# Performance work log

Measured on AMD Instinct MI355X. Metric: run time of the kernel, lower is better.

Reference implementation:

```python
import jax, jax.numpy as jnp
import numpy as np

B, S, H, D = 2, 2048, 16, 64

def setup_inputs() -> dict:
    key = jax.random.key(0)
    kq, kk, kv = jax.random.split(key, 3)
    query = jax.random.normal(kq, (B, S, H, D), dtype=jnp.float32)
    k_ = jax.random.normal(kk, (B, S, H, D), dtype=jnp.float32)
    v_ = jax.random.normal(kv, (B, S, H, D), dtype=jnp.float32)
    return {"query": query, "key": k_, "value": v_}

def reference(query, key, value):
    # AsyncLongContextAttention with world_size=1 degenerates to full
    # softmax attention over the global sequence (all2all / ring are
    # pure data movement). Defaults: causal=False, dropout_p=0.0,
    # softmax_scale = 1/sqrt(head_dim) (flash-attn convention).
    scale = 1.0 / jnp.sqrt(jnp.asarray(query.shape[-1], query.dtype))
    # scores: [B, H, Sq, Sk]
    scores = jnp.einsum("bqhd,bkhd->bhqk", query, key) * scale
    probs = jax.nn.softmax(scores, axis=-1)
    # out: [B, Sq, H, D]
    out = jnp.einsum("bhqk,bkhd->bqhd", probs, value)
    return out
```

## Files before the change

### kernel.cpp

```cpp
#include <hip/hip_runtime.h>
#include <math.h>

using half8  = __attribute__((ext_vector_type(8))) _Float16;
using half4  = __attribute__((ext_vector_type(4))) _Float16;
using fp16x2 = __attribute__((ext_vector_type(2))) __fp16;
using f32x4  = __attribute__((ext_vector_type(4))) float;

namespace {
constexpr int NB = 2, NS = 2048, NH = 16, ND = 64;
constexpr int QBLK = 128, KVBLK = 64;
constexpr int RS = NH * ND;
constexpr int NT = NS / KVBLK;
constexpr int NSTEP = NT / 2;
constexpr size_t TILEH = 4096;
constexpr size_t TILEB = TILEH * 2;
constexpr size_t SCR_HALFS = (size_t)NB * NH * NT * TILEH;

__device__ __forceinline__ int sidx(int row, int col) {
    return row * 64 + (col ^ (((row & 7) ^ ((row >> 3) & 7)) << 3));
}
__device__ __forceinline__ int kperm(int k) {
    return 16 * (2 * (k >> 5) + ((k >> 2) & 1)) + 4 * ((k >> 3) & 3) + (k & 3);
}
__device__ __forceinline__ float ex2(float x) {
#if __has_builtin(__builtin_amdgcn_exp2f)
    return __builtin_amdgcn_exp2f(x);
#else
    return exp2f(x);
#endif
}
__device__ __forceinline__ half8 pk8(const float4& a, const float4& b) {
    half8 r;
    fp16x2* h = (fp16x2*)&r;
    h[0] = __builtin_amdgcn_cvt_pkrtz(a.x, a.y);
    h[1] = __builtin_amdgcn_cvt_pkrtz(a.z, a.w);
    h[2] = __builtin_amdgcn_cvt_pkrtz(b.x, b.y);
    h[3] = __builtin_amdgcn_cvt_pkrtz(b.z, b.w);
    return r;
}
__device__ __forceinline__ half8 pk8s(const float4& a, const float4& b, float s) {
    half8 r;
    fp16x2* h = (fp16x2*)&r;
    h[0] = __builtin_amdgcn_cvt_pkrtz(a.x * s, a.y * s);
    h[1] = __builtin_amdgcn_cvt_pkrtz(a.z * s, a.w * s);
    h[2] = __builtin_amdgcn_cvt_pkrtz(b.x * s, b.y * s);
    h[3] = __builtin_amdgcn_cvt_pkrtz(b.z * s, b.w * s);
    return r;
}
__device__ __forceinline__ half8 pk8v(const float* v) {
    half8 r;
    fp16x2* h = (fp16x2*)&r;
    h[0] = __builtin_amdgcn_cvt_pkrtz(v[0], v[1]);
    h[1] = __builtin_amdgcn_cvt_pkrtz(v[2], v[3]);
    h[2] = __builtin_amdgcn_cvt_pkrtz(v[4], v[5]);
    h[3] = __builtin_amdgcn_cvt_pkrtz(v[6], v[7]);
    return r;
}
__device__ __forceinline__ half8 pkexp(const f32x4& a, const f32x4& b) {
    half8 r;
    fp16x2* h = (fp16x2*)&r;
    h[0] = __builtin_amdgcn_cvt_pkrtz(ex2(a[0]), ex2(a[1]));
    h[1] = __builtin_amdgcn_cvt_pkrtz(ex2(a[2]), ex2(a[3]));
    h[2] = __builtin_amdgcn_cvt_pkrtz(ex2(b[0]), ex2(b[1]));
    h[3] = __builtin_amdgcn_cvt_pkrtz(ex2(b[2]), ex2(b[3]));
    return r;
}
__device__ __forceinline__ void gld16(const void* g, void* l) {
    __builtin_amdgcn_global_load_lds(
        (const __attribute__((address_space(1))) void*)g,
        (__attribute__((address_space(3))) void*)l, 16, 0, 0);
}
}

__global__ __launch_bounds__(512)
void prep_kernel(const float* __restrict__ Kg, const float* __restrict__ Vg,
                 _Float16* __restrict__ Kscr, _Float16* __restrict__ Vscr) {
    const int t  = threadIdx.x;
    const int bh = blockIdx.x;
    const int kt = blockIdx.y;
    const int b  = bh >> 4;
    const int h  = bh & 15;
    const size_t tile = ((size_t)bh * NT + kt) * TILEH;

    {
        const int row = t >> 3;
        const int sc0 = (t & 7) * 8;
        const int m   = kperm(row);
        const int kg  = m >> 4, mlc = m & 15;
        const int ks  = sc0 >> 5, mlg = (sc0 >> 3) & 3;
        const float* kp = Kg + (size_t)(b * NS + kt * KVBLK + row) * RS + h * ND + sc0;
        Kscr[tile + ((ks * 4 + kg) * 64 + mlg * 16 + mlc) * 8 + 0];
        *(half8*)&Kscr[tile + (size_t)((ks * 4 + kg) * 64 + mlg * 16 + mlc) * 8] =
            pk8(*(const float4*)kp, *(const float4*)(kp + 4));
    }

    {
        const int c   = t >> 6;
        const int vl  = t & 63;
        const int vlc = vl & 15, vlg = vl >> 4;
        const int ks  = c >> 2, dg = c & 3;
        const float* vp = Vg + (size_t)(b * NS + kt * KVBLK + 32 * ks + 8 * vlg) * RS
                             + h * ND + 16 * dg + vlc;
        float vv[8];
#pragma unroll
        for (int j = 0; j < 8; ++j) vv[j] = vp[(size_t)j * RS];
        *(half8*)&Vscr[tile + (size_t)(c * 64 + vl) * 8] = pk8v(vv);
    }
}

__global__ __launch_bounds__(512, 4)
void fattn_kernel(const float* __restrict__ Qg, const _Float16* __restrict__ Kscr,
                  const _Float16* __restrict__ Vscr, float* __restrict__ Og) {
    __shared__ __align__(16) _Float16 KT[4][KVBLK * ND];
    __shared__ __align__(16) _Float16 VT[4][KVBLK * ND];
    __shared__ float SL[4 * 2 * 64];

    const int t  = threadIdx.x;
    const int l  = t & 63;
    const int w  = t >> 6;
    const int lc = l & 15;
    const int lg = l >> 4;
    const int parity = w >> 2;
    const int wq = (w & 3) * 32;
    const int bh = blockIdx.x;
    const int qt = blockIdx.y;
    const int b  = bh >> 4;
    const int h  = bh & 15;

    const float SC = 0.18033688011112042f;
    half8 qfr[2][2];
#pragma unroll
    for (int f = 0; f < 2; ++f) {
        const int qrow = qt * QBLK + wq + f * 16 + lc;
        const float* qp = Qg + (size_t)(b * NS + qrow) * RS + h * ND;
#pragma unroll
        for (int ks = 0; ks < 2; ++ks) {
            const float* p = qp + 32 * ks + 8 * lg;
            qfr[f][ks] = pk8s(*(const float4*)p, *(const float4*)(p + 4), SC);
        }
    }

    const f32x4 ZERO = {0.f, 0.f, 0.f, 0.f};
    f32x4 acc[4][2];
    f32x4 lacc0 = ZERO, lacc1 = ZERO;
#pragma unroll
    for (int dg = 0; dg < 4; ++dg) { acc[dg][0] = ZERO; acc[dg][1] = ZERO; }
    half8 ones;
#pragma unroll
    for (int i = 0; i < 8; ++i) ones[i] = (_Float16)1.0f;

    const char* ksrc = (const char*)(Kscr + (size_t)bh * NT * TILEH) + t * 16;
    const char* vsrc = (const char*)(Vscr + (size_t)bh * NT * TILEH) + t * 16;
    const int lofs = l * 8;

    auto STEP = [&](const _Float16* KTb, const _Float16* VTb,
                    _Float16* kA, _Float16* kB, _Float16* vA, _Float16* vB,
                    const char* gkA, const char* gkB,
                    const char* gvA, const char* gvB, bool issue) {
        if (issue) {
            gld16(gkA, kA + w * 512);
            gld16(gkB, kB + w * 512);
            gld16(gvA, vA + w * 512);
            gld16(gvB, vB + w * 512);
        }
        f32x4 st[4][2];
        __builtin_amdgcn_s_setprio(1);
#pragma unroll
        for (int kg = 0; kg < 4; ++kg) {
            const half8 kf = *(const half8*)&KTb[kg * 512 + lofs];
            st[kg][0] = __builtin_amdgcn_mfma_f32_16x16x32_f16(kf, qfr[0][0], ZERO, 0, 0, 0);
            st[kg][1] = __builtin_amdgcn_mfma_f32_16x16x32_f16(kf, qfr[1][0], ZERO, 0, 0, 0);
        }
#pragma unroll
        for (int kg = 0; kg < 4; ++kg) {
            const half8 kf = *(const half8*)&KTb[(4 + kg) * 512 + lofs];
            st[kg][0] = __builtin_amdgcn_mfma_f32_16x16x32_f16(kf, qfr[0][1], st[kg][0], 0, 0, 0);
            st[kg][1] = __builtin_amdgcn_mfma_f32_16x16x32_f16(kf, qfr[1][1], st[kg][1], 0, 0, 0);
        }
        __builtin_amdgcn_s_setprio(0);

        const half8 pA0 = pkexp(st[0][0], st[1][0]);
        const half8 pA1 = pkexp(st[0][1], st[1][1]);
        const half8 pB0 = pkexp(st[2][0], st[3][0]);
        const half8 pB1 = pkexp(st[2][1], st[3][1]);

        lacc0 = __builtin_amdgcn_mfma_f32_16x16x32_f16(ones, pA0, lacc0, 0, 0, 0);
        lacc0 = __builtin_amdgcn_mfma_f32_16x16x32_f16(ones, pB0, lacc0, 0, 0, 0);
        lacc1 = __builtin_amdgcn_mfma_f32_16x16x32_f16(ones, pA1, lacc1, 0, 0, 0);
        lacc1 = __builtin_amdgcn_mfma_f32_16x16x32_f16(ones, pB1, lacc1, 0, 0, 0);

        __builtin_amdgcn_s_setprio(1);
#pragma unroll
        for (int dg = 0; dg < 4; ++dg) {
            const half8 vf0 = *(const half8*)&VTb[dg * 512 + lofs];
            acc[dg][0] = __builtin_amdgcn_mfma_f32_16x16x32_f16(vf0, pA0, acc[dg][0], 0, 0, 0);
            acc[dg][1] = __builtin_amdgcn_mfma_f32_16x16x32_f16(vf0, pA1, acc[dg][1], 0, 0, 0);
        }
#pragma unroll
        for (int dg = 0; dg < 4; ++dg) {
            const half8 vf1 = *(const half8*)&VTb[(4 + dg) * 512 + lofs];
            acc[dg][0] = __builtin_amdgcn_mfma_f32_16x16x32_f16(vf1, pB0, acc[dg][0], 0, 0, 0);
            acc[dg][1] = __builtin_amdgcn_mfma_f32_16x16x32_f16(vf1, pB1, acc[dg][1], 0, 0, 0);
        }
        __builtin_amdgcn_s_setprio(0);
        __syncthreads();
    };

    gld16(ksrc, &KT[0][w * 512]);
    gld16(ksrc + TILEB, &KT[1][w * 512]);
    gld16(vsrc, &VT[0][w * 512]);
    gld16(vsrc + TILEB, &VT[1][w * 512]);
    __syncthreads();

    const char* kcur = ksrc + 2 * TILEB;
    const char* vcur = vsrc + 2 * TILEB;
    for (int s = 0; s < NSTEP; s += 2) {
        STEP(&KT[parity][0], &VT[parity][0],
             &KT[2][0], &KT[3][0], &VT[2][0], &VT[3][0],
             kcur, kcur + TILEB, vcur, vcur + TILEB, true);
        STEP(&KT[2 + parity][0], &VT[2 + parity][0],
             &KT[0][0], &KT[1][0], &VT[0][0], &VT[1][0],
             kcur + 2 * TILEB, kcur + 3 * TILEB,
             vcur + 2 * TILEB, vcur + 3 * TILEB, s + 2 < NSTEP);
        kcur += 4 * TILEB;
        vcur += 4 * TILEB;
    }

    float* sf = (float*)&KT[0][0];
    if (parity) {
        const int uw = w - 4;
#pragma unroll
        for (int dg = 0; dg < 4; ++dg)
#pragma unroll
            for (int f = 0; f < 2; ++f)
                *(float4*)&sf[((uw * 8 + dg * 2 + f) * 64 + l) * 4] = *(float4*)&acc[dg][f];
        SL[(uw * 2 + 0) * 64 + l] = lacc0[0];
        SL[(uw * 2 + 1) * 64 + l] = lacc1[0];
    }
    __syncthreads();
    if (!parity) {
#pragma unroll
        for (int dg = 0; dg < 4; ++dg)
#pragma unroll
            for (int f = 0; f < 2; ++f) {
                const float4 o = *(const float4*)&sf[((w * 8 + dg * 2 + f) * 64 + l) * 4];
                acc[dg][f][0] += o.x; acc[dg][f][1] += o.y;
                acc[dg][f][2] += o.z; acc[dg][f][3] += o.w;
            }
        const float ls[2] = {lacc0[0] + SL[(w * 2 + 0) * 64 + l],
                             lacc1[0] + SL[(w * 2 + 1) * 64 + l]};
#pragma unroll
        for (int f = 0; f < 2; ++f) {
            const float inv  = 1.0f / ls[f];
            const int   qrow = qt * QBLK + wq + f * 16 + lc;
            float* op = Og + (size_t)(b * NS + qrow) * RS + h * ND;
#pragma unroll
            for (int dg = 0; dg < 4; ++dg) {
                float4 o;
                o.x = acc[dg][f][0] * inv;
                o.y = acc[dg][f][1] * inv;
                o.z = acc[dg][f][2] * inv;
                o.w = acc[dg][f][3] * inv;
                *(float4*)(op + 16 * dg + 4 * lg) = o;
            }
        }
    }
}

__global__ __launch_bounds__(512, 4)
void fattn_fb(const float* __restrict__ Qg, const float* __restrict__ Kg,
              const float* __restrict__ Vg, float* __restrict__ Og) {
    __shared__ __align__(16) _Float16 KT[2][KVBLK * ND];
    __shared__ __align__(16) _Float16 VT[2][KVBLK * ND];
    __shared__ __align__(16) _Float16 PS[8][16 * ND];
    const int t = threadIdx.x, l = t & 63, w = t >> 6, lc = l & 15, lg = l >> 4;
    const int bh = blockIdx.x, qt = blockIdx.y, b = bh >> 4, h = bh & 15;
    const float SC = 0.18033688011112042f;
    const int qrow = qt * QBLK + w * 16 + lc;
    half8 qfr[2];
    {
        const float* qp = Qg + (size_t)(b * NS + qrow) * RS + h * ND;
#pragma unroll
        for (int ks = 0; ks < 2; ++ks) {
            const float* p = qp + 32 * ks + 8 * lg;
            qfr[ks] = pk8s(*(const float4*)p, *(const float4*)(p + 4), SC);
        }
    }
    float mrun = -INFINITY, lrun = 0.f;
    const f32x4 zero4 = {0.f, 0.f, 0.f, 0.f};
    f32x4 acc[4];
#pragma unroll
    for (int dg = 0; dg < 4; ++dg) acc[dg] = zero4;
    const int srow = t >> 3, sc0 = (t & 7) * 8;
    const float* kbase = Kg + (size_t)(b * NS) * RS + h * ND + sc0;
    const float* vbase = Vg + (size_t)(b * NS + 8 * w) * RS + h * ND + l;
    float4 kr[2]; float vv[8];
    auto LOAD = [&](int kt) {
        const float* kp = kbase + (size_t)(kt * KVBLK + srow) * RS;
        kr[0] = *(const float4*)(kp + 0);
        kr[1] = *(const float4*)(kp + 4);
        const float* vp = vbase + (size_t)(kt * KVBLK) * RS;
#pragma unroll
        for (int i = 0; i < 8; ++i) vv[i] = vp[(size_t)i * RS];
    };
    auto STORE = [&](int p) {
        *(half8*)&KT[p][sidx(srow, sc0)] = pk8(kr[0], kr[1]);
        *(half8*)&VT[p][sidx(l, 8 * w)]  = pk8v(vv);
    };
    LOAD(0); STORE(0);
    __syncthreads();
    for (int kt = 0; kt < NT; ++kt) {
        const int p = kt & 1;
        if (kt + 1 < NT) LOAD(kt + 1);
        f32x4 st[4];
#pragma unroll
        for (int kg = 0; kg < 4; ++kg) st[kg] = zero4;
#pragma unroll
        for (int ks = 0; ks < 2; ++ks)
#pragma unroll
            for (int kg = 0; kg < 4; ++kg) {
                const half8 kf = *(const half8*)&KT[p][sidx(16 * kg + lc, 32 * ks + 8 * lg)];
                st[kg] = __builtin_amdgcn_mfma_f32_16x16x32_f16(kf, qfr[ks], st[kg], 0, 0, 0);
            }
        {
            float tm = -INFINITY;
#pragma unroll
            for (int kg = 0; kg < 4; ++kg)
#pragma unroll
                for (int r = 0; r < 4; ++r) tm = fmaxf(tm, st[kg][r]);
            tm = fmaxf(tm, __shfl_xor(tm, 16));
            tm = fmaxf(tm, __shfl_xor(tm, 32));
            if (!__all(tm <= mrun)) {
                const float mn = fmaxf(mrun, tm);
                const float corr = exp2f(mrun - mn);
                mrun = mn; lrun *= corr;
#pragma unroll
                for (int dg = 0; dg < 4; ++dg)
#pragma unroll
                    for (int r = 0; r < 4; ++r) acc[dg][r] *= corr;
            }
            float rs = 0.f;
#pragma unroll
            for (int kg = 0; kg < 4; ++kg)
#pragma unroll
                for (int r = 0; r < 4; ++r) {
                    const float pv = exp2f(st[kg][r] - mrun);
                    st[kg][r] = pv; rs += pv;
                }
            rs += __shfl_xor(rs, 16);
            rs += __shfl_xor(rs, 32);
            lrun += rs;
#pragma unroll
            for (int kg = 0; kg < 4; ++kg) {
                half4 ph; fp16x2* hp = (fp16x2*)&ph;
                hp[0] = __builtin_amdgcn_cvt_pkrtz(st[kg][0], st[kg][1]);
                hp[1] = __builtin_amdgcn_cvt_pkrtz(st[kg][2], st[kg][3]);
                *(half4*)&PS[w][sidx(lc, 16 * kg + 4 * lg)] = ph;
            }
        }
#pragma unroll
        for (int ks = 0; ks < 2; ++ks) {
            const half8 pf = *(const half8*)&PS[w][sidx(lc, 32 * ks + 8 * lg)];
#pragma unroll
            for (int dg = 0; dg < 4; ++dg) {
                const half8 vf = *(const half8*)&VT[p][sidx(16 * dg + lc, 32 * ks + 8 * lg)];
                acc[dg] = __builtin_amdgcn_mfma_f32_16x16x32_f16(vf, pf, acc[dg], 0, 0, 0);
            }
        }
        if (kt + 1 < NT) STORE(p ^ 1);
        __syncthreads();
    }
    {
        const float inv = 1.0f / lrun;
        float* op = Og + (size_t)(b * NS + qrow) * RS + h * ND;
#pragma unroll
        for (int dg = 0; dg < 4; ++dg) {
            float4 o;
            o.x = acc[dg][0] * inv; o.y = acc[dg][1] * inv;
            o.z = acc[dg][2] * inv; o.w = acc[dg][3] * inv;
            *(float4*)(op + 16 * dg + 4 * lg) = o;
        }
    }
}

extern "C" void kernel_launch(void* const* d_in, const int* in_sizes, int n_in,
                              void* d_out, int out_size, void* d_ws, size_t ws_size,
                              hipStream_t stream) {
    const float* Q = (const float*)d_in[0];
    const float* K = (const float*)d_in[1];
    const float* V = (const float*)d_in[2];
    float* O = (float*)d_out;
    const size_t need = 2 * SCR_HALFS * sizeof(_Float16);
    if (ws_size >= need) {
        _Float16* Kscr = (_Float16*)d_ws;
        _Float16* Vscr = Kscr + SCR_HALFS;
        prep_kernel<<<dim3(NB * NH, NT), dim3(512), 0, stream>>>(K, V, Kscr, Vscr);
        fattn_kernel<<<dim3(NB * NH, NS / QBLK), dim3(512), 0, stream>>>(Q, Kscr, Vscr, O);
    } else {
        fattn_fb<<<dim3(NB * NH, NS / QBLK), dim3(512), 0, stream>>>(Q, K, V, O);
    }
}
```

Measured before the change: 51.80 us.

## Software-pipeline attention over 32-key tiles with 4-stage LDS ring

```diff
diff --git a/kernel.cpp b/kernel.cpp
--- a/kernel.cpp
+++ b/kernel.cpp
@@ -8,19 +8,20 @@
 
 namespace {
 constexpr int NB = 2, NS = 2048, NH = 16, ND = 64;
-constexpr int QBLK = 128, KVBLK = 64;
+constexpr int QBLK = 128;
+constexpr int KVB = 32;
+constexpr int NTIL = NS / KVB;
+constexpr int NST  = NTIL / 2;
 constexpr int RS = NH * ND;
-constexpr int NT = NS / KVBLK;
-constexpr int NSTEP = NT / 2;
-constexpr size_t TILEH = 4096;
-constexpr size_t TILEB = TILEH * 2;
-constexpr size_t SCR_HALFS = (size_t)NB * NH * NT * TILEH;
+constexpr size_t TIL_H  = 2048;
+constexpr size_t PAIR_B = 8192;
+constexpr size_t SCR_HALFS = (size_t)NB * NH * NTIL * TIL_H;
 
 __device__ __forceinline__ int sidx(int row, int col) {
     return row * 64 + (col ^ (((row & 7) ^ ((row >> 3) & 7)) << 3));
 }
-__device__ __forceinline__ int kperm(int k) {
-    return 16 * (2 * (k >> 5) + ((k >> 2) & 1)) + 4 * ((k >> 3) & 3) + (k & 3);
+__device__ __forceinline__ int kperm32(int k) {
+    return 16 * ((k >> 2) & 1) + 4 * ((k >> 3) & 3) + (k & 3);
 }
 __device__ __forceinline__ float ex2(float x) {
 #if __has_builtin(__builtin_amdgcn_exp2f)
@@ -72,7 +73,7 @@
 }
 }
 
-__global__ __launch_bounds__(512)
+__global__ __launch_bounds__(256)
 void prep_kernel(const float* __restrict__ Kg, const float* __restrict__ Vg,
                  _Float16* __restrict__ Kscr, _Float16* __restrict__ Vscr) {
     const int t  = threadIdx.x;
@@ -80,39 +81,80 @@
     const int kt = blockIdx.y;
     const int b  = bh >> 4;
     const int h  = bh & 15;
-    const size_t tile = ((size_t)bh * NT + kt) * TILEH;
+    const size_t tile = ((size_t)bh * NTIL + kt) * TIL_H;
 
     {
         const int row = t >> 3;
         const int sc0 = (t & 7) * 8;
-        const int m   = kperm(row);
+        const int m   = kperm32(row);
         const int kg  = m >> 4, mlc = m & 15;
         const int ks  = sc0 >> 5, mlg = (sc0 >> 3) & 3;
-        const float* kp = Kg + (size_t)(b * NS + kt * KVBLK + row) * RS + h * ND + sc0;
-        Kscr[tile + ((ks * 4 + kg) * 64 + mlg * 16 + mlc) * 8 + 0];
-        *(half8*)&Kscr[tile + (size_t)((ks * 4 + kg) * 64 + mlg * 16 + mlc) * 8] =
+        const float* kp = Kg + (size_t)(b * NS + kt * KVB + row) * RS + h * ND + sc0;
+        *(half8*)&Kscr[tile + (size_t)((ks * 2 + kg) * 64 + mlg * 16 + mlc) * 8] =
             pk8(*(const float4*)kp, *(const float4*)(kp + 4));
     }
-
     {
         const int c   = t >> 6;
         const int vl  = t & 63;
         const int vlc = vl & 15, vlg = vl >> 4;
-        const int ks  = c >> 2, dg = c & 3;
-        const float* vp = Vg + (size_t)(b * NS + kt * KVBLK + 32 * ks + 8 * vlg) * RS
-                             + h * ND + 16 * dg + vlc;
+        const float* vp = Vg + (size_t)(b * NS + kt * KVB + 8 * vlg) * RS
+                             + h * ND + 16 * c + vlc;
         float vv[8];
 #pragma unroll
         for (int j = 0; j < 8; ++j) vv[j] = vp[(size_t)j * RS];
         *(half8*)&Vscr[tile + (size_t)(c * 64 + vl) * 8] = pk8v(vv);
     }
 }
+
+#define QKT_M(KP, st)                                                              \
+    do {                                                                           \
+        _Pragma("unroll")                                                          \
+        for (int kg = 0; kg < 2; ++kg) {                                           \
+            const half8 kf = *(const half8*)&(KP)[kg * 512 + lofs];                \
+            st[kg][0] = __builtin_amdgcn_mfma_f32_16x16x32_f16(kf, qfr[0][0], ZERO, 0, 0, 0); \
+            st[kg][1] = __builtin_amdgcn_mfma_f32_16x16x32_f16(kf, qfr[1][0], ZERO, 0, 0, 0); \
+        }                                                                          \
+        _Pragma("unroll")                                                          \
+        for (int kg = 0; kg < 2; ++kg) {                                           \
+            const half8 kf = *(const half8*)&(KP)[(2 + kg) * 512 + lofs];          \
+            st[kg][0] = __builtin_amdgcn_mfma_f32_16x16x32_f16(kf, qfr[0][1], st[kg][0], 0, 0, 0); \
+            st[kg][1] = __builtin_amdgcn_mfma_f32_16x16x32_f16(kf, qfr[1][1], st[kg][1], 0, 0, 0); \
+        }                                                                          \
+    } while (0)
+
+#define FIN_M(VP, st)                                                              \
+    do {                                                                           \
+        const half8 pf0 = pkexp(st[0][0], st[1][0]);                               \
+        const half8 pf1 = pkexp(st[0][1], st[1][1]);                               \
+        lacc0 = __builtin_amdgcn_mfma_f32_16x16x32_f16(ones, pf0, lacc0, 0, 0, 0); \
+        lacc1 = __builtin_amdgcn_mfma_f32_16x16x32_f16(ones, pf1, lacc1, 0, 0, 0); \
+        __builtin_amdgcn_s_setprio(1);                                             \
+        _Pragma("unroll")                                                          \
+        for (int dg = 0; dg < 4; ++dg) {                                           \
+            const half8 vf = *(const half8*)&(VP)[dg * 512 + lofs];                \
+            acc[dg][0] = __builtin_amdgcn_mfma_f32_16x16x32_f16(vf, pf0, acc[dg][0], 0, 0, 0); \
+            acc[dg][1] = __builtin_amdgcn_mfma_f32_16x16x32_f16(vf, pf1, acc[dg][1], 0, 0, 0); \
+        }                                                                          \
+        __builtin_amdgcn_s_setprio(0);                                             \
+    } while (0)
+
+#define STAGE_M(j, pairIdx)                                                        \
+    do {                                                                           \
+        gld16(ksrc + (size_t)(pairIdx)*PAIR_B, &SM[j][w * 512]);                   \
+        gld16(vsrc + (size_t)(pairIdx)*PAIR_B, &SM[j][4096 + w * 512]);            \
+    } while (0)
+
+#define BAR2()                                                                     \
+    do {                                                                           \
+        asm volatile("s_waitcnt vmcnt(2)" ::: "memory");                           \
+        __builtin_amdgcn_s_barrier();                                              \
+        __builtin_amdgcn_sched_barrier(0);                                         \
+    } while (0)
 
 __global__ __launch_bounds__(512, 4)
 void fattn_kernel(const float* __restrict__ Qg, const _Float16* __restrict__ Kscr,
                   const _Float16* __restrict__ Vscr, float* __restrict__ Og) {
-    __shared__ __align__(16) _Float16 KT[4][KVBLK * ND];
-    __shared__ __align__(16) _Float16 VT[4][KVBLK * ND];
+    __shared__ __align__(16) _Float16 SM[4][8192];
     __shared__ float SL[4 * 2 * 64];
 
     const int t  = threadIdx.x;
@@ -126,6 +168,7 @@
     const int qt = blockIdx.y;
     const int b  = bh >> 4;
     const int h  = bh & 15;
+    const int lofs = l * 8;
 
     const float SC = 0.18033688011112042f;
     half8 qfr[2][2];
@@ -149,84 +192,61 @@
 #pragma unroll
     for (int i = 0; i < 8; ++i) ones[i] = (_Float16)1.0f;
 
-    const char* ksrc = (const char*)(Kscr + (size_t)bh * NT * TILEH) + t * 16;
-    const char* vsrc = (const char*)(Vscr + (size_t)bh * NT * TILEH) + t * 16;
-    const int lofs = l * 8;
-
-    auto STEP = [&](const _Float16* KTb, const _Float16* VTb,
-                    _Float16* kA, _Float16* kB, _Float16* vA, _Float16* vB,
-                    const char* gkA, const char* gkB,
-                    const char* gvA, const char* gvB, bool issue) {
-        if (issue) {
-            gld16(gkA, kA + w * 512);
-            gld16(gkB, kB + w * 512);
-            gld16(gvA, vA + w * 512);
-            gld16(gvB, vB + w * 512);
-        }
-        f32x4 st[4][2];
-        __builtin_amdgcn_s_setprio(1);
-#pragma unroll
-        for (int kg = 0; kg < 4; ++kg) {
-            const half8 kf = *(const half8*)&KTb[kg * 512 + lofs];
-            st[kg][0] = __builtin_amdgcn_mfma_f32_16x16x32_f16(kf, qfr[0][0], ZERO, 0, 0, 0);
-            st[kg][1] = __builtin_amdgcn_mfma_f32_16x16x32_f16(kf, qfr[1][0], ZERO, 0, 0, 0);
-        }
-#pragma unroll
-        for (int kg = 0; kg < 4; ++kg) {
-            const half8 kf = *(const half8*)&KTb[(4 + kg) * 512 + lofs];
-            st[kg][0] = __builtin_amdgcn_mfma_f32_16x16x32_f16(kf, qfr[0][1], st[kg][0], 0, 0, 0);
-            st[kg][1] = __builtin_amdgcn_mfma_f32_16x16x32_f16(kf, qfr[1][1], st[kg][1], 0, 0, 0);
-        }
-        __builtin_amdgcn_s_setprio(0);
-
-        const half8 pA0 = pkexp(st[0][0], st[1][0]);
-        const half8 pA1 = pkexp(st[0][1], st[1][1]);
-        const half8 pB0 = pkexp(st[2][0], st[3][0]);
-        const half8 pB1 = pkexp(st[2][1], st[3][1]);
-
-        lacc0 = __builtin_amdgcn_mfma_f32_16x16x32_f16(ones, pA0, lacc0, 0, 0, 0);
-        lacc0 = __builtin_amdgcn_mfma_f32_16x16x32_f16(ones, pB0, lacc0, 0, 0, 0);
-        lacc1 = __builtin_amdgcn_mfma_f32_16x16x32_f16(ones, pA1, lacc1, 0, 0, 0);
-        lacc1 = __builtin_amdgcn_mfma_f32_16x16x32_f16(ones, pB1, lacc1, 0, 0, 0);
-
-        __builtin_amdgcn_s_setprio(1);
-#pragma unroll
-        for (int dg = 0; dg < 4; ++dg) {
-            const half8 vf0 = *(const half8*)&VTb[dg * 512 + lofs];
-            acc[dg][0] = __builtin_amdgcn_mfma_f32_16x16x32_f16(vf0, pA0, acc[dg][0], 0, 0, 0);
-            acc[dg][1] = __builtin_amdgcn_mfma_f32_16x16x32_f16(vf0, pA1, acc[dg][1], 0, 0, 0);
-        }
-#pragma unroll
-        for (int dg = 0; dg < 4; ++dg) {
-            const half8 vf1 = *(const half8*)&VTb[(4 + dg) * 512 + lofs];
-            acc[dg][0] = __builtin_amdgcn_mfma_f32_16x16x32_f16(vf1, pB0, acc[dg][0], 0, 0, 0);
-            acc[dg][1] = __builtin_amdgcn_mfma_f32_16x16x32_f16(vf1, pB1, acc[dg][1], 0, 0, 0);
-        }
-        __builtin_amdgcn_s_setprio(0);
-        __syncthreads();
-    };
-
-    gld16(ksrc, &KT[0][w * 512]);
-    gld16(ksrc + TILEB, &KT[1][w * 512]);
-    gld16(vsrc, &VT[0][w * 512]);
-    gld16(vsrc + TILEB, &VT[1][w * 512]);
+    f32x4 stA[2][2], stB[2][2];
+
+    const char* ksrc = (const char*)(Kscr + (size_t)bh * NTIL * TIL_H) + t * 16;
+    const char* vsrc = (const char*)(Vscr + (size_t)bh * NTIL * TIL_H) + t * 16;
+    const _Float16* KB0 = &SM[0][parity * 2048];
+    const _Float16* KB1 = &SM[1][parity * 2048];
+    const _Float16* KB2 = &SM[2][parity * 2048];
+    const _Float16* KB3 = &SM[3][parity * 2048];
+    const _Float16* VB0 = &SM[0][4096 + parity * 2048];
+    const _Float16* VB1 = &SM[1][4096 + parity * 2048];
+    const _Float16* VB2 = &SM[2][4096 + parity * 2048];
+    const _Float16* VB3 = &SM[3][4096 + parity * 2048];
+
+    STAGE_M(0, 0);
+    STAGE_M(1, 1);
+    BAR2();
+    STAGE_M(2, 2);
+    QKT_M(KB0, stA);
+    BAR2();
+    STAGE_M(3, 3);
+    QKT_M(KB1, stB);
+    FIN_M(VB0, stA);
+    BAR2();
+
+    for (int it = 0; it < 7; ++it) {
+        const int p0 = 4 * it + 4;
+        STAGE_M(0, p0);
+        QKT_M(KB2, stA);
+        FIN_M(VB1, stB);
+        BAR2();
+        STAGE_M(1, p0 + 1);
+        QKT_M(KB3, stB);
+        FIN_M(VB2, stA);
+        BAR2();
+        STAGE_M(2, p0 + 2);
+        QKT_M(KB0, stA);
+        FIN_M(VB3, stB);
+        BAR2();
+        STAGE_M(3, p0 + 3);
+        QKT_M(KB1, stB);
+        FIN_M(VB0, stA);
+        BAR2();
+    }
+    QKT_M(KB2, stA);
+    FIN_M(VB1, stB);
+    asm volatile("s_waitcnt vmcnt(0)" ::: "memory");
+    __builtin_amdgcn_s_barrier();
+    __builtin_amdgcn_sched_barrier(0);
+    QKT_M(KB3, stB);
+    FIN_M(VB2, stA);
+    FIN_M(VB3, stB);
+
     __syncthreads();
 
-    const char* kcur = ksrc + 2 * TILEB;
-    const char* vcur = vsrc + 2 * TILEB;
-    for (int s = 0; s < NSTEP; s += 2) {
-        STEP(&KT[parity][0], &VT[parity][0],
-             &KT[2][0], &KT[3][0], &VT[2][0], &VT[3][0],
-             kcur, kcur + TILEB, vcur, vcur + TILEB, true);
-        STEP(&KT[2 + parity][0], &VT[2 + parity][0],
-             &KT[0][0], &KT[1][0], &VT[0][0], &VT[1][0],
-             kcur + 2 * TILEB, kcur + 3 * TILEB,
-             vcur + 2 * TILEB, vcur + 3 * TILEB, s + 2 < NSTEP);
-        kcur += 4 * TILEB;
-        vcur += 4 * TILEB;
-    }
-
-    float* sf = (float*)&KT[0][0];
+    float* sf = (float*)&SM[0][0];
     if (parity) {
         const int uw = w - 4;
 #pragma unroll
@@ -270,6 +290,8 @@
 __global__ __launch_bounds__(512, 4)
 void fattn_fb(const float* __restrict__ Qg, const float* __restrict__ Kg,
               const float* __restrict__ Vg, float* __restrict__ Og) {
+    constexpr int KVBLK = 64;
+    constexpr int NT = NS / KVBLK;
     __shared__ __align__(16) _Float16 KT[2][KVBLK * ND];
     __shared__ __align__(16) _Float16 VT[2][KVBLK * ND];
     __shared__ __align__(16) _Float16 PS[8][16 * ND];
@@ -394,7 +416,7 @@
     if (ws_size >= need) {
         _Float16* Kscr = (_Float16*)d_ws;
         _Float16* Vscr = Kscr + SCR_HALFS;
-        prep_kernel<<<dim3(NB * NH, NT), dim3(512), 0, stream>>>(K, V, Kscr, Vscr);
+        prep_kernel<<<dim3(NB * NH, NTIL), dim3(256), 0, stream>>>(K, V, Kscr, Vscr);
         fattn_kernel<<<dim3(NB * NH, NS / QBLK), dim3(512), 0, stream>>>(Q, Kscr, Vscr, O);
     } else {
         fattn_fb<<<dim3(NB * NH, NS / QBLK), dim3(512), 0, stream>>>(Q, K, V, O);
```

Measured after the change: 52.23 us. No clear change (+0.8%).
